# Kernel optimization log

Hardware: AMD Instinct MI355X
Metric: run time of the kernel (lower is better)

## Reference

```python
import jax, jax.numpy as jnp
import numpy as np
from jax import lax

H = 512
V = 32000
B = 64
S = 64
T = 32
TQ = 32
NUM_HOP = 3


def _p(key, shape, scale=0.05):
    return jax.random.normal(key, shape, dtype=jnp.float32) * scale


def setup_inputs() -> dict:
    key = jax.random.key(0)
    ks = jax.random.split(key, 20)
    inp = {}
    inp["contexts"] = jax.random.randint(ks[0], (B, S, T), 0, V)
    inp["questions"] = jax.random.randint(ks[1], (B, TQ), 0, V)
    inp["emb"] = _p(ks[2], (V, H), 1.0)
    # input module: bidirectional GRU (torch gate order r,z,n)
    inp["Wih_f"] = _p(ks[3], (3 * H, H)); inp["Whh_f"] = _p(ks[4], (3 * H, H))
    inp["bih_f"] = jnp.zeros((3 * H,), jnp.float32); inp["bhh_f"] = jnp.zeros((3 * H,), jnp.float32)
    inp["Wih_b"] = _p(ks[5], (3 * H, H)); inp["Whh_b"] = _p(ks[6], (3 * H, H))
    inp["bih_b"] = jnp.zeros((3 * H,), jnp.float32); inp["bhh_b"] = jnp.zeros((3 * H,), jnp.float32)
    # question module GRU
    inp["qWih"] = _p(ks[7], (3 * H, H)); inp["qWhh"] = _p(ks[8], (3 * H, H))
    inp["qbih"] = jnp.zeros((3 * H,), jnp.float32); inp["qbhh"] = jnp.zeros((3 * H,), jnp.float32)
    # attention GRU cell (note: source reuses br as both biases)
    inp["Wr"] = _p(ks[9], (H, H)); inp["Ur"] = _p(ks[10], (H, H)); inp["br"] = jnp.ones((H,), jnp.float32)
    inp["W"] = _p(ks[11], (H, H)); inp["U"] = _p(ks[12], (H, H))
    # episodic memory gate MLP + next-memory projection
    inp["z1_w"] = _p(ks[13], (H, 4 * H)); inp["z1_b"] = jnp.zeros((H,), jnp.float32)
    inp["z2_w"] = _p(ks[14], (1, H)); inp["z2_b"] = jnp.zeros((1,), jnp.float32)
    inp["nm_w"] = _p(ks[15], (H, 3 * H)); inp["nm_b"] = jnp.zeros((H,), jnp.float32)
    # answer module
    inp["ans_w"] = _p(ks[16], (V, 2 * H)); inp["ans_b"] = jnp.zeros((V,), jnp.float32)
    return inp


def _pos_enc(slen, elen):
    # l[s, e] = 1 - s/slen - (e/elen)*(1 - 2*s/slen); indexed by SENTENCE dim, as in source
    s = np.arange(slen, dtype=np.float64)[:, None]
    e = np.arange(elen, dtype=np.float64)[None, :]
    l = 1.0 - s / slen - (e / elen) * (1.0 - 2.0 * s / slen)
    return jnp.asarray(l, dtype=jnp.float32)  # (S, H)


def _gru(x, Wih, Whh, bih, bhh, reverse=False):
    # x: (B, T, H); torch nn.GRU math with gate order r, z, n
    Bn, Tn, Hn = x.shape
    h0 = jnp.zeros((Bn, Hn), x.dtype)

    def step(h, xt):
        gx = xt @ Wih.T + bih
        gh = h @ Whh.T + bhh
        xr, xz, xn = jnp.split(gx, 3, axis=-1)
        hr, hz, hn = jnp.split(gh, 3, axis=-1)
        r = jax.nn.sigmoid(xr + hr)
        z = jax.nn.sigmoid(xz + hz)
        n = jnp.tanh(xn + r * hn)
        h_new = (1.0 - z) * n + z * h
        return h_new, h_new

    h_last, hs = lax.scan(step, h0, jnp.swapaxes(x, 0, 1), reverse=reverse)
    return jnp.swapaxes(hs, 0, 1), h_last


def _dmn(emb, Wih_f, Whh_f, bih_f, bhh_f, Wih_b, Whh_b, bih_b, bhh_b,
         qWih, qWhh, qbih, qbhh, Wr, Ur, br, W, U,
         z1_w, z1_b, z2_w, z2_b, nm_w, nm_b, ans_w, ans_b,
         contexts, questions):
    emb0 = emb.at[0].set(0.0)  # padding_idx=0
    Bn, Sn, Tn = contexts.shape
    Hn = emb.shape[1]
    # ---- input module ----
    ce = emb0[contexts]                                   # (B,S,T,H)
    pe = _pos_enc(Sn, Hn)                                 # (S,H), broadcast over tokens (faithful)
    facts_in = jnp.sum(ce * pe[None, :, None, :], axis=2)  # (B,S,H)
    hf, _ = _gru(facts_in, Wih_f, Whh_f, bih_f, bhh_f, reverse=False)
    hb, _ = _gru(facts_in, Wih_b, Whh_b, bih_b, bhh_b, reverse=True)
    facts = hf + hb                                       # (B,S,H); dropout = identity (eval)
    # ---- question module ----
    _, q = _gru(emb0[questions], qWih, qWhh, qbih, qbhh)  # (B,H)
    # ---- episodic memory hops ----
    facts_t = jnp.swapaxes(facts, 0, 1)                   # (S,B,H)
    M = q
    for _ in range(NUM_HOP):
        qb = q[:, None, :]
        Mb = M[:, None, :]
        z = jnp.concatenate([facts * qb, facts * Mb,
                             jnp.abs(facts - qb), jnp.abs(facts - Mb)], axis=-1)  # (B,S,4H)
        g1 = jnp.tanh(z @ z1_w.T + z1_b)
        G = jax.nn.softmax((g1 @ z2_w.T + z2_b)[..., 0], axis=1)  # (B,S)

        def agru(c, sg):
            fact, g = sg
            r = jax.nn.sigmoid(fact @ Wr + c @ Ur + br)
            ht = jnp.tanh(fact @ W + r * (c @ U) + br)  # source reuses br as b
            return g[:, None] * ht + (1.0 - g[:, None]) * c, None

        C, _ = lax.scan(agru, jnp.zeros((Bn, Hn), facts.dtype), (facts_t, G.T))
        M = jax.nn.relu(jnp.concatenate([M, C, q], axis=-1) @ nm_w.T + nm_b)
    # ---- answer module (dropout = identity) ----
    preds = jnp.concatenate([M, q], axis=-1) @ ans_w.T + ans_b  # (B,V)
    return preds


def reference(contexts, questions, emb, Wih_f, Whh_f, bih_f, bhh_f,
              Wih_b, Whh_b, bih_b, bhh_b, qWih, qWhh, qbih, qbhh,
              Wr, Ur, br, W, U, z1_w, z1_b, z2_w, z2_b, nm_w, nm_b,
              ans_w, ans_b):
    return _dmn(emb, Wih_f, Whh_f, bih_f, bhh_f, Wih_b, Whh_b, bih_b, bhh_b,
                qWih, qWhh, qbih, qbhh, Wr, Ur, br, W, U,
                z1_w, z1_b, z2_w, z2_b, nm_w, nm_b, ans_w, ans_b,
                contexts, questions)
```

## Files before the change

kernel.cpp:

```cpp
#include <hip/hip_runtime.h>
#include <cstddef>
#include <cstdint>

namespace {

constexpr int H  = 512;
constexpr int V  = 32000;
constexpr int B  = 64;
constexpr int S  = 64;
constexpr int T  = 32;
constexpr int TQ = 32;

typedef unsigned short ushort_t;
typedef __attribute__((ext_vector_type(8))) short bf16x8;
typedef __attribute__((ext_vector_type(4))) short bf16x4;
typedef __attribute__((ext_vector_type(4))) float f32x4;
typedef __attribute__((ext_vector_type(4))) unsigned u32x4;

__device__ __forceinline__ ushort_t f2bf(float f) {
  union { float f; unsigned u; } v; v.f = f;
  return (ushort_t)((v.u + 0x7FFFu + ((v.u >> 16) & 1u)) >> 16);
}

__device__ __forceinline__ float sigm(float x) { return 1.f / (1.f + expf(-x)); }

__device__ __forceinline__ bf16x8 pack8(f32x4 a, f32x4 b) {
  bf16x8 r;
  r[0] = (short)f2bf(a[0]); r[1] = (short)f2bf(a[1]);
  r[2] = (short)f2bf(a[2]); r[3] = (short)f2bf(a[3]);
  r[4] = (short)f2bf(b[0]); r[5] = (short)f2bf(b[1]);
  r[6] = (short)f2bf(b[2]); r[7] = (short)f2bf(b[3]);
  return r;
}

__device__ __forceinline__ u32x4 ld16c(const void* p) {
  u32x4 v;
  asm volatile("global_load_dwordx4 %0, %1, off sc0 sc1" : "=v"(v) : "v"(p));
  return v;
}
__device__ __forceinline__ void st2c(ushort_t* p, unsigned v) {
  asm volatile("global_store_short %0, %1, off sc0 sc1" :: "v"(p), "v"(v) : "memory");
}
__device__ __forceinline__ void stflag(unsigned* p, unsigned v) {
  asm volatile("global_store_dword %0, %1, off sc0 sc1" :: "v"(p), "v"(v) : "memory");
}
__device__ __forceinline__ unsigned ldflag(const unsigned* p) {
  unsigned v;
  asm volatile("global_load_dword %0, %1, off sc0 sc1" : "=v"(v) : "v"(p));
  return v;
}
__device__ __forceinline__ void waitvm0() {
  asm volatile("s_waitcnt vmcnt(0)" ::: "memory");
  __builtin_amdgcn_sched_barrier(0);
}

__global__ __launch_bounds__(256) void k_embed_facts(const int* __restrict__ ctx,
                                                     const float* __restrict__ emb,
                                                     float* __restrict__ facts_in) {
  const int bs = blockIdx.x;
  const int s  = bs & (S - 1);
  const int t  = threadIdx.x;
  __shared__ int sidx[T];
  if (t < T) sidx[t] = ctx[(size_t)bs * T + t];
  __syncthreads();
  float a0 = 0.f, a1 = 0.f;
  for (int tt = 0; tt < T; ++tt) {
    const int ix = sidx[tt];
    if (ix != 0) {
      const float* e = emb + ((size_t)ix << 9);
      a0 += e[t];
      a1 += e[t + 256];
    }
  }
  const float sf = (float)s * (1.f / 64.f);
  const float c1 = 1.f - sf;
  const float c2 = (1.f - 2.f * sf) * (1.f / 512.f);
  facts_in[((size_t)bs << 9) + t]       = a0 * (c1 - (float)t * c2);
  facts_in[((size_t)bs << 9) + t + 256] = a1 * (c1 - (float)(t + 256) * c2);
}

__global__ __launch_bounds__(256) void k_embed_q(const int* __restrict__ qidx,
                                                 const float* __restrict__ emb,
                                                 float* __restrict__ qe) {
  const int bt = blockIdx.x;
  const int t  = threadIdx.x;
  const int ix = qidx[bt];
  float v0 = 0.f, v1 = 0.f;
  if (ix != 0) {
    const float* e = emb + ((size_t)ix << 9);
    v0 = e[t];
    v1 = e[t + 256];
  }
  qe[((size_t)bt << 9) + t]       = v0;
  qe[((size_t)bt << 9) + t + 256] = v1;
}

__global__ __launch_bounds__(256) void k_transpose512(const float* __restrict__ src,
                                                      float* __restrict__ dst) {
  __shared__ float tile[32][33];
  const int x0 = blockIdx.x * 32, y0 = blockIdx.y * 32;
  for (int i = threadIdx.y; i < 32; i += 8)
    tile[i][threadIdx.x] = src[(size_t)(y0 + i) * H + x0 + threadIdx.x];
  __syncthreads();
  for (int i = threadIdx.y; i < 32; i += 8)
    dst[(size_t)(x0 + i) * H + y0 + threadIdx.x] = tile[threadIdx.x][i];
}

template <bool A_BF16, int ACT>
__global__ __launch_bounds__(256) void k_gemm_mfma(const void* __restrict__ Av,
                                                   const float* __restrict__ Bm,
                                                   const float* __restrict__ bias,
                                                   float* __restrict__ C,
                                                   int M, int N, int K) {
  __shared__ __align__(16) ushort_t As[64][72];
  __shared__ __align__(16) ushort_t Bs[64][72];
  const int t    = threadIdx.x;
  const int lane = t & 63;
  const int w    = t >> 6;
  const int wr   = w >> 1, wc = w & 1;
  const int m0 = blockIdx.y << 6, n0 = blockIdx.x << 6;
  const int row = t >> 2;
  const int ch  = t & 3;

  f32x4 acc[2][2] = {};

  for (int k0 = 0; k0 < K; k0 += 64) {
    if (A_BF16) {
      const ushort_t* A16 = (const ushort_t*)Av;
#pragma unroll
      for (int cc = 0; cc < 2; ++cc) {
        const int c8 = ch + cc * 4;
        const uint4 v = *(const uint4*)(A16 + (size_t)(m0 + row) * K + k0 + c8 * 8);
        *(uint4*)&As[row][c8 * 8] = v;
      }
    } else {
      const float* Af = (const float*)Av;
#pragma unroll
      for (int cc = 0; cc < 2; ++cc) {
        const int c8 = ch + cc * 4;
        const float* src = Af + (size_t)(m0 + row) * K + k0 + c8 * 8;
        *(bf16x8*)&As[row][c8 * 8] = pack8(*(const f32x4*)src, *(const f32x4*)(src + 4));
      }
    }
#pragma unroll
    for (int cc = 0; cc < 2; ++cc) {
      const int c8 = ch + cc * 4;
      const float* srb = Bm + (size_t)(n0 + row) * K + k0 + c8 * 8;
      *(bf16x8*)&Bs[row][c8 * 8] = pack8(*(const f32x4*)srb, *(const f32x4*)(srb + 4));
    }
    __syncthreads();
#pragma unroll
    for (int ks = 0; ks < 2; ++ks) {
      bf16x8 a[2], b[2];
#pragma unroll
      for (int fr = 0; fr < 2; ++fr)
        a[fr] = *(const bf16x8*)&As[wr * 32 + fr * 16 + (lane & 15)][ks * 32 + (lane >> 4) * 8];
#pragma unroll
      for (int fc = 0; fc < 2; ++fc)
        b[fc] = *(const bf16x8*)&Bs[wc * 32 + fc * 16 + (lane & 15)][ks * 32 + (lane >> 4) * 8];
#pragma unroll
      for (int fr = 0; fr < 2; ++fr)
#pragma unroll
        for (int fc = 0; fc < 2; ++fc)
          acc[fr][fc] = __builtin_amdgcn_mfma_f32_16x16x32_bf16(a[fr], b[fc], acc[fr][fc], 0, 0, 0);
    }
    __syncthreads();
  }
#pragma unroll
  for (int fr = 0; fr < 2; ++fr) {
#pragma unroll
    for (int fc = 0; fc < 2; ++fc) {
      const int rbase = m0 + wr * 32 + fr * 16 + ((lane >> 4) << 2);
      const int col   = n0 + wc * 32 + fc * 16 + (lane & 15);
      const float bv  = bias ? bias[col] : 0.f;
#pragma unroll
      for (int j = 0; j < 4; ++j) {
        float v = acc[fr][fc][j] + bv;
        if (ACT == 1) v = tanhf(v);
        if (ACT == 2) v = fmaxf(v, 0.f);
        C[(size_t)(rbase + j) * N + col] = v;
      }
    }
  }
}

__global__ __launch_bounds__(256) void k_build_z16(const float* __restrict__ facts,
                                                   const float* __restrict__ q,
                                                   const float* __restrict__ M,
                                                   ushort_t* __restrict__ z) {
  const int bs = blockIdx.x;
  const int b  = bs >> 6;
  const int t  = threadIdx.x;
  const size_t zb = (size_t)bs << 11;
  for (int c = t; c < 512; c += 256) {
    const float f  = facts[((size_t)bs << 9) + c];
    const float qv = q[(b << 9) + c];
    const float mv = M[(b << 9) + c];
    z[zb + c]        = f2bf(f * qv);
    z[zb + 512 + c]  = f2bf(f * mv);
    z[zb + 1024 + c] = f2bf(fabsf(f - qv));
    z[zb + 1536 + c] = f2bf(fabsf(f - mv));
  }
}

__global__ __launch_bounds__(256) void k_gemm_cat3(const float* __restrict__ Mv,
                                                   const float* __restrict__ Cv,
                                                   const float* __restrict__ qv,
                                                   const float* __restrict__ Bm,
                                                   const float* __restrict__ bias,
                                                   float* __restrict__ C) {
  constexpr int N = 512, K = 1536;
  __shared__ __align__(16) ushort_t As[64][72];
  __shared__ __align__(16) ushort_t Bs[64][72];
  const int t    = threadIdx.x;
  const int lane = t & 63;
  const int w    = t >> 6;
  const int wr   = w >> 1, wc = w & 1;
  const int n0 = blockIdx.x << 6;
  const int row = t >> 2;
  const int ch  = t & 3;

  f32x4 acc[2][2] = {};

  for (int k0 = 0; k0 < K; k0 += 64) {
    const int seg = k0 >> 9;
    const float* src = (seg == 0) ? Mv : (seg == 1) ? Cv : qv;
    const int kb = k0 & 511;
#pragma unroll
    for (int cc = 0; cc < 2; ++cc) {
      const int c8 = ch + cc * 4;
      const float* fp = src + ((size_t)row << 9) + kb + c8 * 8;
      *(bf16x8*)&As[row][c8 * 8] = pack8(*(const f32x4*)fp, *(const f32x4*)(fp + 4));
      const float* srb = Bm + (size_t)(n0 + row) * K + k0 + c8 * 8;
      *(bf16x8*)&Bs[row][c8 * 8] = pack8(*(const f32x4*)srb, *(const f32x4*)(srb + 4));
    }
    __syncthreads();
#pragma unroll
    for (int ks = 0; ks < 2; ++ks) {
      bf16x8 a[2], bb[2];
#pragma unroll
      for (int fr = 0; fr < 2; ++fr)
        a[fr] = *(const bf16x8*)&As[wr * 32 + fr * 16 + (lane & 15)][ks * 32 + (lane >> 4) * 8];
#pragma unroll
      for (int fc = 0; fc < 2; ++fc)
        bb[fc] = *(const bf16x8*)&Bs[wc * 32 + fc * 16 + (lane & 15)][ks * 32 + (lane >> 4) * 8];
#pragma unroll
      for (int fr = 0; fr < 2; ++fr)
#pragma unroll
        for (int fc = 0; fc < 2; ++fc)
          acc[fr][fc] = __builtin_amdgcn_mfma_f32_16x16x32_bf16(a[fr], bb[fc], acc[fr][fc], 0, 0, 0);
    }
    __syncthreads();
  }
#pragma unroll
  for (int fr = 0; fr < 2; ++fr) {
#pragma unroll
    for (int fc = 0; fc < 2; ++fc) {
      const int rbase = wr * 32 + fr * 16 + ((lane >> 4) << 2);
      const int col   = n0 + wc * 32 + fc * 16 + (lane & 15);
      const float bv  = bias[col];
#pragma unroll
      for (int j = 0; j < 4; ++j)
        C[(size_t)(rbase + j) * N + col] = fmaxf(acc[fr][fc][j] + bv, 0.f);
    }
  }
}

__global__ __launch_bounds__(256) void k_gemm_cat2(const float* __restrict__ Mv,
                                                   const float* __restrict__ qv,
                                                   const float* __restrict__ Bm,
                                                   const float* __restrict__ bias,
                                                   float* __restrict__ C) {
  constexpr int N = 32000, K = 1024;
  __shared__ __align__(16) ushort_t As[64][72];
  __shared__ __align__(16) ushort_t Bs[64][72];
  const int t    = threadIdx.x;
  const int lane = t & 63;
  const int w    = t >> 6;
  const int wr   = w >> 1, wc = w & 1;
  const int n0 = blockIdx.x << 6;
  const int row = t >> 2;
  const int ch  = t & 3;

  f32x4 acc[2][2] = {};

  for (int k0 = 0; k0 < K; k0 += 64) {
    const float* src = (k0 < 512) ? Mv : qv;
    const int kb = k0 & 511;
#pragma unroll
    for (int cc = 0; cc < 2; ++cc) {
      const int c8 = ch + cc * 4;
      const float* fp = src + ((size_t)row << 9) + kb + c8 * 8;
      *(bf16x8*)&As[row][c8 * 8] = pack8(*(const f32x4*)fp, *(const f32x4*)(fp + 4));
      const float* srb = Bm + (size_t)(n0 + row) * K + k0 + c8 * 8;
      *(bf16x8*)&Bs[row][c8 * 8] = pack8(*(const f32x4*)srb, *(const f32x4*)(srb + 4));
    }
    __syncthreads();
#pragma unroll
    for (int ks = 0; ks < 2; ++ks) {
      bf16x8 a[2], bb[2];
#pragma unroll
      for (int fr = 0; fr < 2; ++fr)
        a[fr] = *(const bf16x8*)&As[wr * 32 + fr * 16 + (lane & 15)][ks * 32 + (lane >> 4) * 8];
#pragma unroll
      for (int fc = 0; fc < 2; ++fc)
        bb[fc] = *(const bf16x8*)&Bs[wc * 32 + fc * 16 + (lane & 15)][ks * 32 + (lane >> 4) * 8];
#pragma unroll
      for (int fr = 0; fr < 2; ++fr)
#pragma unroll
        for (int fc = 0; fc < 2; ++fc)
          acc[fr][fc] = __builtin_amdgcn_mfma_f32_16x16x32_bf16(a[fr], bb[fc], acc[fr][fc], 0, 0, 0);
    }
    __syncthreads();
  }
#pragma unroll
  for (int fr = 0; fr < 2; ++fr) {
#pragma unroll
    for (int fc = 0; fc < 2; ++fc) {
      const int rbase = wr * 32 + fr * 16 + ((lane >> 4) << 2);
      const int col   = n0 + wc * 32 + fc * 16 + (lane & 15);
      const float bv  = bias[col];
#pragma unroll
      for (int j = 0; j < 4; ++j)
        C[(size_t)(rbase + j) * N + col] = acc[fr][fc][j] + bv;
    }
  }
}

__global__ __launch_bounds__(256, 1) void k_gru_scan_mfma(
    const float* __restrict__ Whh_f, const float* __restrict__ bhh_f,
    const float* __restrict__ Whh_b, const float* __restrict__ bhh_b,
    const float* __restrict__ qWhh,  const float* __restrict__ qbhh,
    const float* __restrict__ gx_f, const float* __restrict__ gx_b,
    const float* __restrict__ gx_q,
    ushort_t* __restrict__ H16, float* __restrict__ qbuf,
    float* __restrict__ facts, float* __restrict__ hb_all,
    unsigned* __restrict__ flags_base) {
  const int bx   = blockIdx.x;
  const int grp  = bx >> 3;
  const int rank = bx & 7;
  const int gru  = grp >> 2;
  const int ib   = grp & 3;

  const float* Whh; const float* bhh; const float* gx;
  float* out_seq; int seqlen, rev;
  if (gru == 0)      { Whh = Whh_f; bhh = bhh_f; gx = gx_f; out_seq = facts;   seqlen = S;  rev = 0; }
  else if (gru == 1) { Whh = Whh_b; bhh = bhh_b; gx = gx_b; out_seq = hb_all;  seqlen = S;  rev = 1; }
  else               { Whh = qWhh;  bhh = qbhh;  gx = gx_q; out_seq = nullptr; seqlen = TQ; rev = 0; }
  ushort_t* Hb0 = H16 + gru * 65536;
  ushort_t* Hb1 = Hb0 + 32768;

  __shared__ __align__(16) ushort_t hl[16 * 520];

  const int t    = threadIdx.x;
  const int lane = t & 63;
  const int wv   = t >> 6;
  const int nt   = (rank << 2) + wv;
  const int lm   = lane & 15;
  const int lk   = lane >> 4;
  const int col  = (nt << 4) + lm;

  bf16x8 wf[3][16];
#pragma unroll
  for (int g = 0; g < 3; ++g) {
    const float* wrow = Whh + ((size_t)(g * 512 + col) << 9) + (lk << 3);
#pragma unroll
    for (int ks = 0; ks < 16; ++ks) {
      const float* p = wrow + ks * 32;
      wf[g][ks] = pack8(*(const f32x4*)p, *(const f32x4*)(p + 4));
    }
  }
  const float bv0 = bhh[col], bv1 = bhh[512 + col], bv2 = bhh[1024 + col];
  unsigned* flags = flags_base + grp * 8 * 32;

  float xr[4], xz[4], xn[4];
  {
    const int xidx = rev ? (seqlen - 1) : 0;
#pragma unroll
    for (int j = 0; j < 4; ++j) {
      const int b = (ib << 4) + (lk << 2) + j;
      const size_t gxrow = ((size_t)b * seqlen + xidx) * 1536;
      xr[j] = gx[gxrow + col];
      xz[j] = gx[gxrow + 512 + col];
      xn[j] = gx[gxrow + 1024 + col];
    }
  }

  float hp[4] = {0.f, 0.f, 0.f, 0.f};

  for (int s = 0; s < seqlen; ++s) {
    if (s == 0) {
      for (int i = t; i < 4160; i += 256) ((unsigned*)hl)[i] = 0u;
    } else {
      const ushort_t* Hp16 = (s & 1) ? Hb1 : Hb0;
      u32x4 v[4];
#pragma unroll
      for (int u = 0; u < 4; ++u) {
        const int i = (u << 8) + t;
        v[u] = ld16c(Hp16 + ((size_t)((ib << 4) + (i >> 6)) << 9) + ((i << 3) & 511));
      }
      waitvm0();
#pragma unroll
      for (int u = 0; u < 4; ++u) {
        const int i = (u << 8) + t;
        *(u32x4*)&hl[(i >> 6) * 520 + ((i << 3) & 511)] = v[u];
      }
    }
    __syncthreads();

    f32x4 acc0 = {}, acc1 = {}, acc2 = {};
#pragma unroll
    for (int ks = 0; ks < 16; ++ks) {
      const bf16x8 a = *(const bf16x8*)&hl[lm * 520 + (ks << 5) + (lk << 3)];
      acc0 = __builtin_amdgcn_mfma_f32_16x16x32_bf16(a, wf[0][ks], acc0, 0, 0, 0);
      acc1 = __builtin_amdgcn_mfma_f32_16x16x32_bf16(a, wf[1][ks], acc1, 0, 0, 0);
      acc2 = __builtin_amdgcn_mfma_f32_16x16x32_bf16(a, wf[2][ks], acc2, 0, 0, 0);
    }

    const int xidx = rev ? (seqlen - 1 - s) : s;
    ushort_t* Hn16 = (s & 1) ? Hb0 : Hb1;
    float hn4[4];
#pragma unroll
    for (int j = 0; j < 4; ++j) {
      const int b = (ib << 4) + (lk << 2) + j;
      const float r = sigm(xr[j] + acc0[j] + bv0);
      const float z = sigm(xz[j] + acc1[j] + bv1);
      const float n = tanhf(xn[j] + r * (acc2[j] + bv2));
      const float hnew = (1.f - z) * n + z * hp[j];
      hp[j] = hnew;
      hn4[j] = hnew;
      if (s + 1 < seqlen) st2c(Hn16 + ((size_t)b << 9) + col, (unsigned)f2bf(hnew));
    }

    if (s + 1 < seqlen) {
      waitvm0();
      __syncthreads();
      if (t == 0) stflag(flags + rank * 32, (unsigned)(s + 1));
#pragma unroll
      for (int j = 0; j < 4; ++j) {
        const int b = (ib << 4) + (lk << 2) + j;
        if (out_seq) out_seq[((size_t)(b * S + xidx) << 9) + col] = hn4[j];
      }
      const int xidx2 = rev ? (seqlen - 2 - s) : (s + 1);
      float nxr[4], nxz[4], nxn[4];
#pragma unroll
      for (int j = 0; j < 4; ++j) {
        const int b = (ib << 4) + (lk << 2) + j;
        const size_t gxrow = ((size_t)b * seqlen + xidx2) * 1536;
        nxr[j] = gx[gxrow + col];
        nxz[j] = gx[gxrow + 512 + col];
        nxn[j] = gx[gxrow + 1024 + col];
      }
      if (wv == 0) {
        const unsigned* fp = flags + (lane & 7) * 32;
        for (;;) {
          const unsigned v = ldflag(fp);
          asm volatile("s_waitcnt vmcnt(0)" ::: "memory");
          const int ok = (lane >= 8) || (v >= (unsigned)(s + 1));
          if (__all(ok)) break;
          __builtin_amdgcn_s_sleep(1);
        }
      }
      __syncthreads();
#pragma unroll
      for (int j = 0; j < 4; ++j) { xr[j] = nxr[j]; xz[j] = nxz[j]; xn[j] = nxn[j]; }
    } else {
#pragma unroll
      for (int j = 0; j < 4; ++j) {
        const int b = (ib << 4) + (lk << 2) + j;
        if (out_seq) out_seq[((size_t)(b * S + xidx) << 9) + col] = hn4[j];
        if (gru == 2) qbuf[((size_t)b << 9) + col] = hn4[j];
      }
    }
  }
}

__global__ __launch_bounds__(256, 1) void k_agru_scan_mfma(
    const float* __restrict__ UrT, const float* __restrict__ UT,
    const float* __restrict__ fRW, const float* __restrict__ fW,
    const float* __restrict__ br, const float* __restrict__ G,
    ushort_t* __restrict__ C16, float* __restrict__ C0f,
    unsigned* __restrict__ flags_base) {
  const int bx   = blockIdx.x;
  const int grp  = bx >> 3;
  const int rank = bx & 7;
  ushort_t* Cb0 = C16;
  ushort_t* Cb1 = C16 + 32768;

  __shared__ __align__(16) ushort_t cl[16 * 520];

  const int t    = threadIdx.x;
  const int lane = t & 63;
  const int wv   = t >> 6;
  const int nt   = (rank << 2) + wv;
  const int lm   = lane & 15;
  const int lk   = lane >> 4;
  const int col  = (nt << 4) + lm;

  bf16x8 wfr[16], wfu[16];
  {
    const float* r0 = UrT + ((size_t)col << 9) + (lk << 3);
    const float* r1 = UT  + ((size_t)col << 9) + (lk << 3);
#pragma unroll
    for (int ks = 0; ks < 16; ++ks) {
      wfr[ks] = pack8(*(const f32x4*)(r0 + ks * 32), *(const f32x4*)(r0 + ks * 32 + 4));
      wfu[ks] = pack8(*(const f32x4*)(r1 + ks * 32), *(const f32x4*)(r1 + ks * 32 + 4));
    }
  }
  const float brv = br[col];
  unsigned* flags = flags_base + grp * 8 * 32;

  float fr[4], fw[4], gg[4];
#pragma unroll
  for (int j = 0; j < 4; ++j) {
    const int b = (grp << 4) + (lk << 2) + j;
    const size_t fi = ((size_t)(b * S) << 9) + col;
    fr[j] = fRW[fi];
    fw[j] = fW[fi];
    gg[j] = G[b << 6];
  }

  float cp[4] = {0.f, 0.f, 0.f, 0.f};

  for (int s = 0; s < S; ++s) {
    if (s == 0) {
      for (int i = t; i < 4160; i += 256) ((unsigned*)cl)[i] = 0u;
    } else {
      const ushort_t* Cp16 = (s & 1) ? Cb1 : Cb0;
      u32x4 v[4];
#pragma unroll
      for (int u = 0; u < 4; ++u) {
        const int i = (u << 8) + t;
        v[u] = ld16c(Cp16 + ((size_t)((grp << 4) + (i >> 6)) << 9) + ((i << 3) & 511));
      }
      waitvm0();
#pragma unroll
      for (int u = 0; u < 4; ++u) {
        const int i = (u << 8) + t;
        *(u32x4*)&cl[(i >> 6) * 520 + ((i << 3) & 511)] = v[u];
      }
    }
    __syncthreads();

    f32x4 accr = {}, accu = {};
#pragma unroll
    for (int ks = 0; ks < 16; ++ks) {
      const bf16x8 a = *(const bf16x8*)&cl[lm * 520 + (ks << 5) + (lk << 3)];
      accr = __builtin_amdgcn_mfma_f32_16x16x32_bf16(a, wfr[ks], accr, 0, 0, 0);
      accu = __builtin_amdgcn_mfma_f32_16x16x32_bf16(a, wfu[ks], accu, 0, 0, 0);
    }

    ushort_t* Cn16 = (s & 1) ? Cb0 : Cb1;
    float cn4[4];
#pragma unroll
    for (int j = 0; j < 4; ++j) {
      const int b = (grp << 4) + (lk << 2) + j;
      const float r  = sigm(fr[j] + accr[j] + brv);
      const float ht = tanhf(fw[j] + r * accu[j] + brv);
      const float cnew = gg[j] * ht + (1.f - gg[j]) * cp[j];
      cp[j] = cnew;
      cn4[j] = cnew;
      if (s + 1 < S) st2c(Cn16 + ((size_t)b << 9) + col, (unsigned)f2bf(cnew));
    }

    if (s + 1 < S) {
      waitvm0();
      __syncthreads();
      if (t == 0) stflag(flags + rank * 32, (unsigned)(s + 1));
      float nfr[4], nfw[4], ngg[4];
#pragma unroll
      for (int j = 0; j < 4; ++j) {
        const int b = (grp << 4) + (lk << 2) + j;
        const size_t fi = ((size_t)(b * S + s + 1) << 9) + col;
        nfr[j] = fRW[fi];
        nfw[j] = fW[fi];
        ngg[j] = G[(b << 6) + s + 1];
      }
      if (wv == 0) {
        const unsigned* fp = flags + (lane & 7) * 32;
        for (;;) {
          const unsigned v = ldflag(fp);
          asm volatile("s_waitcnt vmcnt(0)" ::: "memory");
          const int ok = (lane >= 8) || (v >= (unsigned)(s + 1));
          if (__all(ok)) break;
          __builtin_amdgcn_s_sleep(1);
        }
      }
      __syncthreads();
#pragma unroll
      for (int j = 0; j < 4; ++j) { fr[j] = nfr[j]; fw[j] = nfw[j]; gg[j] = ngg[j]; }
    } else {
#pragma unroll
      for (int j = 0; j < 4; ++j) {
        const int b = (grp << 4) + (lk << 2) + j;
        C0f[((size_t)b << 9) + col] = cn4[j];
      }
    }
  }
}

__global__ __launch_bounds__(256) void k_add(float* __restrict__ a, const float* __restrict__ b) {
  const size_t i = (((size_t)blockIdx.x << 8) + threadIdx.x) << 2;
  float4 x = *(float4*)(a + i);
  const float4 y = *(const float4*)(b + i);
  x.x += y.x; x.y += y.y; x.z += y.z; x.w += y.w;
  *(float4*)(a + i) = x;
}

__global__ __launch_bounds__(256) void k_score_softmax(const float* __restrict__ g1,
                                                       const float* __restrict__ z2w,
                                                       const float* __restrict__ z2b,
                                                       float* __restrict__ G) {
  const int b = blockIdx.x, t = threadIdx.x;
  const int wave = t >> 6, lane = t & 63;
  __shared__ float sc[64];
  for (int si = 0; si < 16; ++si) {
    const int s = wave * 16 + si;
    const float* row = g1 + ((size_t)(b * S + s) << 9) + lane * 8;
    const float* w   = z2w + lane * 8;
    float p = 0.f;
#pragma unroll
    for (int k = 0; k < 8; ++k) p += row[k] * w[k];
#pragma unroll
    for (int off = 32; off; off >>= 1) p += __shfl_xor(p, off);
    if (lane == 0) sc[s] = p + z2b[0];
  }
  __syncthreads();
  if (wave == 0) {
    const float v = sc[lane];
    float m = v;
#pragma unroll
    for (int off = 32; off; off >>= 1) m = fmaxf(m, __shfl_xor(m, off));
    const float e = expf(v - m);
    float su = e;
#pragma unroll
    for (int off = 32; off; off >>= 1) su += __shfl_xor(su, off);
    G[(b << 6) + lane] = e / su;
  }
}

}

extern "C" void kernel_launch(void* const* d_in, const int* in_sizes, int n_in,
                              void* d_out, int out_size, void* d_ws, size_t ws_size,
                              hipStream_t stream) {
  const int*   contexts  = (const int*)d_in[0];
  const int*   questions = (const int*)d_in[1];
  const float* emb   = (const float*)d_in[2];
  const float* Wih_f = (const float*)d_in[3];
  const float* Whh_f = (const float*)d_in[4];
  const float* bih_f = (const float*)d_in[5];
  const float* bhh_f = (const float*)d_in[6];
  const float* Wih_b = (const float*)d_in[7];
  const float* Whh_b = (const float*)d_in[8];
  const float* bih_b = (const float*)d_in[9];
  const float* bhh_b = (const float*)d_in[10];
  const float* qWih  = (const float*)d_in[11];
  const float* qWhh  = (const float*)d_in[12];
  const float* qbih  = (const float*)d_in[13];
  const float* qbhh  = (const float*)d_in[14];
  const float* Wr    = (const float*)d_in[15];
  const float* Ur    = (const float*)d_in[16];
  const float* br    = (const float*)d_in[17];
  const float* Wm    = (const float*)d_in[18];
  const float* Um    = (const float*)d_in[19];
  const float* z1_w  = (const float*)d_in[20];
  const float* z1_b  = (const float*)d_in[21];
  const float* z2_w  = (const float*)d_in[22];
  const float* z2_b  = (const float*)d_in[23];
  const float* nm_w  = (const float*)d_in[24];
  const float* nm_b  = (const float*)d_in[25];
  const float* ans_w = (const float*)d_in[26];
  const float* ans_b = (const float*)d_in[27];
  (void)in_sizes; (void)n_in; (void)out_size; (void)ws_size;

  float* ws = (float*)d_ws;
  float* WrT      = ws + 0;
  float* UrT      = ws + 262144;
  float* WT       = ws + 524288;
  float* UT       = ws + 786432;
  float* facts_in = ws + 1048576;
  float* qe       = ws + 3145728;
  float* gx_f     = ws + 4194304;
  float* gx_b     = ws + 10485760;
  float* gx_q     = ws + 16777216;
  float* facts    = ws + 19922944;
  float* hb       = ws + 22020096;
  float* Hbuf     = ws + 24117248;
  float* C0       = ws + 24313856;
  float* M0       = ws + 24379392;
  float* M1       = ws + 24412160;
  float* Mq       = ws + 24543232;
  float* Gm       = ws + 24608768;
  ushort_t* H16 = (ushort_t*)Hbuf;
  float* qbuf   = Hbuf + 98304;
  ushort_t* C16 = (ushort_t*)(Hbuf + 131072);
  ushort_t* zb16 = (ushort_t*)gx_f;
  float* g1  = gx_q;
  float* fRW = facts_in;
  float* fW  = hb;
  float* preds = (float*)d_out;
  unsigned* bar = (unsigned*)Mq;
  float* q = qbuf;

  hipMemsetAsync(bar, 0, 6144 * sizeof(unsigned), stream);

  k_embed_facts<<<B * S, 256, 0, stream>>>(contexts, emb, facts_in);
  k_embed_q<<<B * TQ, 256, 0, stream>>>(questions, emb, qe);
  dim3 tb(32, 8);
  k_transpose512<<<dim3(16, 16), tb, 0, stream>>>(Wr, WrT);
  k_transpose512<<<dim3(16, 16), tb, 0, stream>>>(Ur, UrT);
  k_transpose512<<<dim3(16, 16), tb, 0, stream>>>(Wm, WT);
  k_transpose512<<<dim3(16, 16), tb, 0, stream>>>(Um, UT);

  k_gemm_mfma<false, 0><<<dim3(24, 64), 256, 0, stream>>>(facts_in, Wih_f, bih_f, gx_f, 4096, 1536, 512);
  k_gemm_mfma<false, 0><<<dim3(24, 64), 256, 0, stream>>>(facts_in, Wih_b, bih_b, gx_b, 4096, 1536, 512);
  k_gemm_mfma<false, 0><<<dim3(24, 32), 256, 0, stream>>>(qe, qWih, qbih, gx_q, 2048, 1536, 512);

  k_gru_scan_mfma<<<96, 256, 0, stream>>>(Whh_f, bhh_f, Whh_b, bhh_b, qWhh, qbhh,
                                          gx_f, gx_b, gx_q, H16, qbuf, facts, hb, bar);
  k_add<<<2048, 256, 0, stream>>>(facts, hb);

  k_gemm_mfma<false, 0><<<dim3(8, 64), 256, 0, stream>>>(facts, WrT, nullptr, fRW, 4096, 512, 512);
  k_gemm_mfma<false, 0><<<dim3(8, 64), 256, 0, stream>>>(facts, WT,  nullptr, fW,  4096, 512, 512);

  const float* Mcur = q;
  for (int h = 0; h < 3; ++h) {
    k_build_z16<<<B * S, 256, 0, stream>>>(facts, q, Mcur, zb16);
    k_gemm_mfma<true, 1><<<dim3(8, 64), 256, 0, stream>>>(zb16, z1_w, z1_b, g1, 4096, 512, 2048);
    k_score_softmax<<<B, 256, 0, stream>>>(g1, z2_w, z2_b, Gm);
    unsigned* fl = bar + 3072 + h * 1024;
    k_agru_scan_mfma<<<32, 256, 0, stream>>>(UrT, UT, fRW, fW, br, Gm, C16, C0, fl);
    float* Mnext = (h & 1) ? M1 : M0;
    k_gemm_cat3<<<dim3(8, 1), 256, 0, stream>>>(Mcur, C0, q, nm_w, nm_b, Mnext);
    Mcur = Mnext;
  }

  k_gemm_cat2<<<dim3(500, 1), 256, 0, stream>>>(Mcur, q, ans_w, ans_b, preds);
}
```

Before: 1.362 ms.

## Hoist hop-invariant question half of gate GEMM and batch projection GEMMs

Splits the z1 gate weight into question-dependent and memory-dependent halves. The question half (facts*q, |facts-q|) is computed once before the hop loop, and each hop only runs a K=1024 GEMM on the memory half, adding the cached partial before tanh. The three GRU input-projection GEMMs are also merged into one launch, as are the two facts projections. This halves the per-hop gate GEMM work and cuts launch count, at the cost of extra workspace buffers and one weight-split kernel.

```diff
diff --git a/kernel.cpp b/kernel.cpp
--- a/kernel.cpp
+++ b/kernel.cpp
@@ -106,12 +106,59 @@
     dst[(size_t)(x0 + i) * H + y0 + threadIdx.x] = tile[threadIdx.x][i];
 }
 
-template <bool A_BF16, int ACT>
+__global__ __launch_bounds__(256) void k_split_z1w(const float* __restrict__ z1w,
+                                                   float* __restrict__ Bq,
+                                                   float* __restrict__ Bm) {
+  const int n = blockIdx.x;
+  const int t = threadIdx.x;
+  const float* src = z1w + (size_t)n * 2048;
+  float* dq = Bq + (size_t)n * 1024;
+  float* dm = Bm + (size_t)n * 1024;
+  for (int k = t; k < 512; k += 256) {
+    dq[k]       = src[k];
+    dq[512 + k] = src[1024 + k];
+    dm[k]       = src[512 + k];
+    dm[512 + k] = src[1536 + k];
+  }
+}
+
+__global__ __launch_bounds__(256) void k_build_zq16(const float* __restrict__ facts,
+                                                    const float* __restrict__ q,
+                                                    ushort_t* __restrict__ zq) {
+  const int bs = blockIdx.x;
+  const int b  = bs >> 6;
+  const int t  = threadIdx.x;
+  const size_t zb = (size_t)bs << 10;
+  for (int c = t; c < 512; c += 256) {
+    const float f  = facts[((size_t)bs << 9) + c];
+    const float qv = q[(b << 9) + c];
+    zq[zb + c]       = f2bf(f * qv);
+    zq[zb + 512 + c] = f2bf(fabsf(f - qv));
+  }
+}
+
+__global__ __launch_bounds__(256) void k_build_zm16(const float* __restrict__ facts,
+                                                    const float* __restrict__ M,
+                                                    ushort_t* __restrict__ zm) {
+  const int bs = blockIdx.x;
+  const int b  = bs >> 6;
+  const int t  = threadIdx.x;
+  const size_t zb = (size_t)bs << 10;
+  for (int c = t; c < 512; c += 256) {
+    const float f  = facts[((size_t)bs << 9) + c];
+    const float mv = M[(b << 9) + c];
+    zm[zb + c]       = f2bf(f * mv);
+    zm[zb + 512 + c] = f2bf(fabsf(f - mv));
+  }
+}
+
+template <bool A_BF16, int ACT, bool ADDC>
 __global__ __launch_bounds__(256) void k_gemm_mfma(const void* __restrict__ Av,
                                                    const float* __restrict__ Bm,
                                                    const float* __restrict__ bias,
                                                    float* __restrict__ C,
-                                                   int M, int N, int K) {
+                                                   int M, int N, int K,
+                                                   const float* __restrict__ Cin) {
   __shared__ __align__(16) ushort_t As[64][72];
   __shared__ __align__(16) ushort_t Bs[64][72];
   const int t    = threadIdx.x;
@@ -176,6 +223,7 @@
 #pragma unroll
       for (int j = 0; j < 4; ++j) {
         float v = acc[fr][fc][j] + bv;
+        if (ADDC) v += Cin[(size_t)(rbase + j) * N + col];
         if (ACT == 1) v = tanhf(v);
         if (ACT == 2) v = fmaxf(v, 0.f);
         C[(size_t)(rbase + j) * N + col] = v;
@@ -184,22 +232,131 @@
   }
 }
 
-__global__ __launch_bounds__(256) void k_build_z16(const float* __restrict__ facts,
-                                                   const float* __restrict__ q,
-                                                   const float* __restrict__ M,
-                                                   ushort_t* __restrict__ z) {
-  const int bs = blockIdx.x;
-  const int b  = bs >> 6;
-  const int t  = threadIdx.x;
-  const size_t zb = (size_t)bs << 11;
-  for (int c = t; c < 512; c += 256) {
-    const float f  = facts[((size_t)bs << 9) + c];
-    const float qv = q[(b << 9) + c];
-    const float mv = M[(b << 9) + c];
-    z[zb + c]        = f2bf(f * qv);
-    z[zb + 512 + c]  = f2bf(f * mv);
-    z[zb + 1024 + c] = f2bf(fabsf(f - qv));
-    z[zb + 1536 + c] = f2bf(fabsf(f - mv));
+__global__ __launch_bounds__(256) void k_gemm_b3(
+    const float* __restrict__ facts_in, const float* __restrict__ qe,
+    const float* __restrict__ Wih_f, const float* __restrict__ bih_f,
+    const float* __restrict__ Wih_b, const float* __restrict__ bih_b,
+    const float* __restrict__ qWih,  const float* __restrict__ qbih,
+    float* __restrict__ gx_f, float* __restrict__ gx_b, float* __restrict__ gx_q) {
+  constexpr int N = 1536, K = 512;
+  const int y = blockIdx.y;
+  const float* Af; const float* Bw; const float* bias; float* C; int m0;
+  if (y < 64)       { Af = facts_in; Bw = Wih_f; bias = bih_f; C = gx_f; m0 = y << 6; }
+  else if (y < 128) { Af = facts_in; Bw = Wih_b; bias = bih_b; C = gx_b; m0 = (y - 64) << 6; }
+  else              { Af = qe;       Bw = qWih;  bias = qbih;  C = gx_q; m0 = (y - 128) << 6; }
+
+  __shared__ __align__(16) ushort_t As[64][72];
+  __shared__ __align__(16) ushort_t Bs[64][72];
+  const int t    = threadIdx.x;
+  const int lane = t & 63;
+  const int w    = t >> 6;
+  const int wr   = w >> 1, wc = w & 1;
+  const int n0 = blockIdx.x << 6;
+  const int row = t >> 2;
+  const int ch  = t & 3;
+
+  f32x4 acc[2][2] = {};
+
+  for (int k0 = 0; k0 < K; k0 += 64) {
+#pragma unroll
+    for (int cc = 0; cc < 2; ++cc) {
+      const int c8 = ch + cc * 4;
+      const float* src = Af + (size_t)(m0 + row) * K + k0 + c8 * 8;
+      *(bf16x8*)&As[row][c8 * 8] = pack8(*(const f32x4*)src, *(const f32x4*)(src + 4));
+      const float* srb = Bw + (size_t)(n0 + row) * K + k0 + c8 * 8;
+      *(bf16x8*)&Bs[row][c8 * 8] = pack8(*(const f32x4*)srb, *(const f32x4*)(srb + 4));
+    }
+    __syncthreads();
+#pragma unroll
+    for (int ks = 0; ks < 2; ++ks) {
+      bf16x8 a[2], b[2];
+#pragma unroll
+      for (int fr = 0; fr < 2; ++fr)
+        a[fr] = *(const bf16x8*)&As[wr * 32 + fr * 16 + (lane & 15)][ks * 32 + (lane >> 4) * 8];
+#pragma unroll
+      for (int fc = 0; fc < 2; ++fc)
+        b[fc] = *(const bf16x8*)&Bs[wc * 32 + fc * 16 + (lane & 15)][ks * 32 + (lane >> 4) * 8];
+#pragma unroll
+      for (int fr = 0; fr < 2; ++fr)
+#pragma unroll
+        for (int fc = 0; fc < 2; ++fc)
+          acc[fr][fc] = __builtin_amdgcn_mfma_f32_16x16x32_bf16(a[fr], b[fc], acc[fr][fc], 0, 0, 0);
+    }
+    __syncthreads();
+  }
+#pragma unroll
+  for (int fr = 0; fr < 2; ++fr) {
+#pragma unroll
+    for (int fc = 0; fc < 2; ++fc) {
+      const int rbase = m0 + wr * 32 + fr * 16 + ((lane >> 4) << 2);
+      const int col   = n0 + wc * 32 + fc * 16 + (lane & 15);
+      const float bv  = bias[col];
+#pragma unroll
+      for (int j = 0; j < 4; ++j)
+        C[(size_t)(rbase + j) * N + col] = acc[fr][fc][j] + bv;
+    }
+  }
+}
+
+__global__ __launch_bounds__(256) void k_gemm_d2(
+    const float* __restrict__ facts,
+    const float* __restrict__ WrT, const float* __restrict__ WT,
+    float* __restrict__ fRW, float* __restrict__ fW) {
+  constexpr int N = 512, K = 512;
+  const int y = blockIdx.y;
+  const float* Bw = (y < 64) ? WrT : WT;
+  float* C = (y < 64) ? fRW : fW;
+  const int m0 = (y & 63) << 6;
+
+  __shared__ __align__(16) ushort_t As[64][72];
+  __shared__ __align__(16) ushort_t Bs[64][72];
+  const int t    = threadIdx.x;
+  const int lane = t & 63;
+  const int w    = t >> 6;
+  const int wr   = w >> 1, wc = w & 1;
+  const int n0 = blockIdx.x << 6;
+  const int row = t >> 2;
+  const int ch  = t & 3;
+
+  f32x4 acc[2][2] = {};
+
+  for (int k0 = 0; k0 < K; k0 += 64) {
+#pragma unroll
+    for (int cc = 0; cc < 2; ++cc) {
+      const int c8 = ch + cc * 4;
+      const float* src = facts + (size_t)(m0 + row) * K + k0 + c8 * 8;
+      *(bf16x8*)&As[row][c8 * 8] = pack8(*(const f32x4*)src, *(const f32x4*)(src + 4));
+      const float* srb = Bw + (size_t)(n0 + row) * K + k0 + c8 * 8;
+      *(bf16x8*)&Bs[row][c8 * 8] = pack8(*(const f32x4*)srb, *(const f32x4*)(srb + 4));
+    }
+    __syncthreads();
+#pragma unroll
+    for (int ks = 0; ks < 2; ++ks) {
+      bf16x8 a[2], b[2];
+#pragma unroll
+      for (int fr = 0; fr < 2; ++fr)
+        a[fr] = *(const bf16x8*)&As[wr * 32 + fr * 16 + (lane & 15)][ks * 32 + (lane >> 4) * 8];
+#pragma unroll
+      for (int fc = 0; fc < 2; ++fc)
+        b[fc] = *(const bf16x8*)&Bs[wc * 32 + fc * 16 + (lane & 15)][ks * 32 + (lane >> 4) * 8];
+#pragma unroll
+      for (int fr = 0; fr < 2; ++fr)
+#pragma unroll
+        for (int fc = 0; fc < 2; ++fc)
+          acc[fr][fc] = __builtin_amdgcn_mfma_f32_16x16x32_bf16(a[fr], b[fc], acc[fr][fc], 0, 0, 0);
+    }
+    __syncthreads();
+  }
+#pragma unroll
+  for (int fr = 0; fr < 2; ++fr) {
+#pragma unroll
+    for (int fc = 0; fc < 2; ++fc) {
+      const int rbase = m0 + wr * 32 + fr * 16 + ((lane >> 4) << 2);
+      const int col   = n0 + wc * 32 + fc * 16 + (lane & 15);
+#pragma unroll
+      for (int j = 0; j < 4; ++j)
+        C[(size_t)(rbase + j) * N + col] = acc[fr][fc][j];
+    }
   }
 }
 
@@ -695,7 +852,11 @@
   ushort_t* H16 = (ushort_t*)Hbuf;
   float* qbuf   = Hbuf + 98304;
   ushort_t* C16 = (ushort_t*)(Hbuf + 131072);
-  ushort_t* zb16 = (ushort_t*)gx_f;
+  ushort_t* zq16 = (ushort_t*)gx_f;
+  ushort_t* zm16 = (ushort_t*)(gx_f + 2097152);
+  float* g1q = gx_f + 4194304;
+  float* Bq  = gx_b;
+  float* Bmw = gx_b + 524288;
   float* g1  = gx_q;
   float* fRW = facts_in;
   float* fW  = hb;
@@ -713,21 +874,25 @@
   k_transpose512<<<dim3(16, 16), tb, 0, stream>>>(Wm, WT);
   k_transpose512<<<dim3(16, 16), tb, 0, stream>>>(Um, UT);
 
-  k_gemm_mfma<false, 0><<<dim3(24, 64), 256, 0, stream>>>(facts_in, Wih_f, bih_f, gx_f, 4096, 1536, 512);
-  k_gemm_mfma<false, 0><<<dim3(24, 64), 256, 0, stream>>>(facts_in, Wih_b, bih_b, gx_b, 4096, 1536, 512);
-  k_gemm_mfma<false, 0><<<dim3(24, 32), 256, 0, stream>>>(qe, qWih, qbih, gx_q, 2048, 1536, 512);
+  k_gemm_b3<<<dim3(24, 160), 256, 0, stream>>>(facts_in, qe, Wih_f, bih_f,
+                                               Wih_b, bih_b, qWih, qbih,
+                                               gx_f, gx_b, gx_q);
 
   k_gru_scan_mfma<<<96, 256, 0, stream>>>(Whh_f, bhh_f, Whh_b, bhh_b, qWhh, qbhh,
                                           gx_f, gx_b, gx_q, H16, qbuf, facts, hb, bar);
   k_add<<<2048, 256, 0, stream>>>(facts, hb);
 
-  k_gemm_mfma<false, 0><<<dim3(8, 64), 256, 0, stream>>>(facts, WrT, nullptr, fRW, 4096, 512, 512);
-  k_gemm_mfma<false, 0><<<dim3(8, 64), 256, 0, stream>>>(facts, WT,  nullptr, fW,  4096, 512, 512);
+  k_split_z1w<<<512, 256, 0, stream>>>(z1_w, Bq, Bmw);
+  k_build_zq16<<<B * S, 256, 0, stream>>>(facts, q, zq16);
+  k_gemm_d2<<<dim3(8, 128), 256, 0, stream>>>(facts, WrT, WT, fRW, fW);
+  k_gemm_mfma<true, 0, false><<<dim3(8, 64), 256, 0, stream>>>(zq16, Bq, nullptr, g1q,
+                                                               4096, 512, 1024, nullptr);
 
   const float* Mcur = q;
   for (int h = 0; h < 3; ++h) {
-    k_build_z16<<<B * S, 256, 0, stream>>>(facts, q, Mcur, zb16);
-    k_gemm_mfma<true, 1><<<dim3(8, 64), 256, 0, stream>>>(zb16, z1_w, z1_b, g1, 4096, 512, 2048);
+    k_build_zm16<<<B * S, 256, 0, stream>>>(facts, Mcur, zm16);
+    k_gemm_mfma<true, 1, true><<<dim3(8, 64), 256, 0, stream>>>(zm16, Bmw, z1_b, g1,
+                                                                4096, 512, 1024, g1q);
     k_score_softmax<<<B, 256, 0, stream>>>(g1, z2_w, z2_b, Gm);
     unsigned* fl = bar + 3072 + h * 1024;
     k_agru_scan_mfma<<<32, 256, 0, stream>>>(UrT, UT, fRW, fW, br, Gm, C16, C0, fl);
```

New measurement: 1.330 ms. 1.02x faster.
